# Kernel tuning notes

Hardware: AMD Instinct MI355X
Metric: run time of the kernel (lower is better)

## Reference

```python
import jax, jax.numpy as jnp
import numpy as np

B = 100000          # polymers
MOLS_PER = 4        # 3 monomers + 1 solvent per polymer
N = B * MOLS_PER
D = 64              # rdkit feature dim
F = 64              # polymer-level feature dim
H = 128             # hidden dim


def setup_inputs() -> dict:
    key = jax.random.key(0)
    ks = jax.random.split(key, 6)
    polymer_feats = jax.random.normal(ks[0], (B, F), dtype=jnp.float32)
    rdkit = jax.random.normal(ks[1], (N, D), dtype=jnp.float32)
    # sorted segment ids; last molecule of each segment is the solvent
    polymer_mapping = jnp.repeat(jnp.arange(B, dtype=jnp.int32), MOLS_PER)
    W1 = jax.random.normal(ks[2], (F + 2 * D, H), dtype=jnp.float32) * 0.05
    b1 = jnp.zeros((H,), jnp.float32)
    W2 = jax.random.normal(ks[3], (H, H // 2), dtype=jnp.float32) * 0.05
    b2 = jnp.zeros((H // 2,), jnp.float32)
    W3 = jax.random.normal(ks[4], (H // 2, 1), dtype=jnp.float32) * 0.05
    b3 = jnp.zeros((1,), jnp.float32)
    return {"polymer_feats": polymer_feats, "rdkit": rdkit,
            "polymer_mapping": polymer_mapping,
            "W1": W1, "b1": b1, "W2": W2, "b2": b2, "W3": W3, "b3": b3}


def _combine_rdkit(rdkit, polymer_mapping, num_polymers):
    # solvent = last row of each consecutive segment
    last = jnp.concatenate([polymer_mapping[1:] != polymer_mapping[:-1],
                            jnp.ones((1,), dtype=bool)])
    mono = ~last
    mono_w = mono.astype(rdkit.dtype)
    mono_sum = jax.ops.segment_sum(rdkit * mono_w[:, None], polymer_mapping,
                                   num_segments=num_polymers)
    mono_cnt = jax.ops.segment_sum(mono_w, polymer_mapping,
                                   num_segments=num_polymers)
    mono_avg = mono_sum / mono_cnt[:, None]
    solvent = jax.ops.segment_sum(rdkit * last.astype(rdkit.dtype)[:, None],
                                  polymer_mapping, num_segments=num_polymers)
    return jnp.concatenate([mono_avg, solvent], axis=1)  # [B, 2D]


def reference(polymer_feats, rdkit, polymer_mapping, W1, b1, W2, b2, W3, b3):
    num_polymers = polymer_feats.shape[0]
    pooled = _combine_rdkit(rdkit, polymer_mapping, num_polymers)
    x = jnp.concatenate([polymer_feats, pooled], axis=1)  # [B, F+2D]
    h = jax.nn.relu(x @ W1 + b1)          # dropout is identity in eval mode
    h = jax.nn.relu(h @ W2 + b2)
    return h @ W3 + b3                    # [B, 1]
```

## Files before the change

### kernel.cpp

```cpp
#include <hip/hip_runtime.h>

#define BPOLY  100000
#define TILE_M 64
#define NBLK   ((BPOLY + TILE_M - 1) / TILE_M)
#define KSTR   200

typedef __attribute__((ext_vector_type(8))) _Float16 f16x8;
typedef __attribute__((ext_vector_type(4))) _Float16 f16x4;
typedef __attribute__((ext_vector_type(4))) float    f32x4;

#define W1T 0
#define W2T 24576

__global__ __launch_bounds__(256) void prep_weights(
    const float* __restrict__ W1,
    const float* __restrict__ W2,
    _Float16* __restrict__ ws) {
  int i = blockIdx.x * 256 + threadIdx.x;
  if (i < 24576) {
    int k = i >> 7, n = i & 127;
    ws[W1T + n * 192 + k] = (_Float16)W1[i];
  } else {
    int j = i - 24576;
    int k = j >> 6, n = j & 63;
    ws[W2T + n * 128 + k] = (_Float16)W2[j];
  }
}

__global__ __launch_bounds__(256, 6) void fnn_mfma(
    const float* __restrict__ pf,
    const float* __restrict__ rdkit,
    const _Float16* __restrict__ ws,
    const float* __restrict__ b1,
    const float* __restrict__ b2,
    const float* __restrict__ W3,
    const float* __restrict__ b3,
    float* __restrict__ out) {
  __shared__ __align__(16) _Float16 Xs[64 * KSTR];

  const int tid  = threadIdx.x;
  const int p0   = blockIdx.x * TILE_M;
  const int lane = tid & 63;
  const int wv   = tid >> 6;
  const int lmod = lane & 15;
  const int lq   = lane >> 4;

  #pragma unroll
  for (int i = 0; i < 4; ++i) {
    int f = tid + i * 256;
    int m = f >> 4, kq = (f & 15) * 4;
    float4 v = make_float4(0.f, 0.f, 0.f, 0.f);
    if (p0 + m < BPOLY) v = *(const float4*)(pf + (size_t)(p0 + m) * 64 + kq);
    f16x4 h = {(_Float16)v.x, (_Float16)v.y, (_Float16)v.z, (_Float16)v.w};
    *(f16x4*)&Xs[m * KSTR + kq] = h;
  }
  #pragma unroll
  for (int i = 0; i < 4; ++i) {
    int f = tid + i * 256;
    int m = f >> 4, kq = (f & 15) * 4;
    float4 r0 = {0,0,0,0}, r1 = {0,0,0,0}, r2 = {0,0,0,0}, r3 = {0,0,0,0};
    if (p0 + m < BPOLY) {
      const float* base = rdkit + (size_t)(p0 + m) * 256 + kq;
      r0 = *(const float4*)(base);
      r1 = *(const float4*)(base + 64);
      r2 = *(const float4*)(base + 128);
      r3 = *(const float4*)(base + 192);
    }
    const float inv3 = 1.0f / 3.0f;
    f16x4 av = {(_Float16)((r0.x + r1.x + r2.x) * inv3),
                (_Float16)((r0.y + r1.y + r2.y) * inv3),
                (_Float16)((r0.z + r1.z + r2.z) * inv3),
                (_Float16)((r0.w + r1.w + r2.w) * inv3)};
    f16x4 sv = {(_Float16)r3.x, (_Float16)r3.y, (_Float16)r3.z, (_Float16)r3.w};
    *(f16x4*)&Xs[m * KSTR + 64 + kq]  = av;
    *(f16x4*)&Xs[m * KSTR + 128 + kq] = sv;
  }
  __syncthreads();

  const float b1v0 = b1[32 * wv + lmod];
  const float b1v1 = b1[32 * wv + 16 + lmod];
  const _Float16* w1t = ws + W1T;
  const int bcol0 = (32 * wv + lmod) * 192;
  const int bcol1 = (32 * wv + 16 + lmod) * 192;

  f32x4 acc1[4][2];
  #pragma unroll
  for (int mt = 0; mt < 4; ++mt) {
    acc1[mt][0] = (f32x4){0.f, 0.f, 0.f, 0.f};
    acc1[mt][1] = (f32x4){0.f, 0.f, 0.f, 0.f};
  }

  #pragma unroll 2
  for (int ks = 0; ks < 6; ++ks) {
    const int ko = ks * 32 + lq * 8;
    f16x8 b0 = *(const f16x8*)(w1t + bcol0 + ko);
    f16x8 b1f = *(const f16x8*)(w1t + bcol1 + ko);
    #pragma unroll
    for (int mt = 0; mt < 4; ++mt) {
      f16x8 a = *(const f16x8*)&Xs[(mt * 16 + lmod) * KSTR + ko];
      acc1[mt][0] = __builtin_amdgcn_mfma_f32_16x16x32_f16(a, b0,  acc1[mt][0], 0, 0, 0);
      acc1[mt][1] = __builtin_amdgcn_mfma_f32_16x16x32_f16(a, b1f, acc1[mt][1], 0, 0, 0);
    }
  }
  __syncthreads();

  #pragma unroll
  for (int mt = 0; mt < 4; ++mt) {
    #pragma unroll
    for (int nn = 0; nn < 2; ++nn) {
      const float bv = nn ? b1v1 : b1v0;
      const int col = 32 * wv + 16 * nn + lmod;
      #pragma unroll
      for (int r = 0; r < 4; ++r) {
        float h = fmaxf(acc1[mt][nn][r] + bv, 0.f);
        Xs[(mt * 16 + lq * 4 + r) * KSTR + col] = (_Float16)h;
      }
    }
  }
  __syncthreads();

  const float b2v = b2[16 * wv + lmod];
  const float w3v = W3[16 * wv + lmod];
  const _Float16* w2t = ws + W2T;
  const int bcol2 = (16 * wv + lmod) * 128;

  f32x4 acc2[4];
  #pragma unroll
  for (int mt = 0; mt < 4; ++mt) acc2[mt] = (f32x4){0.f, 0.f, 0.f, 0.f};

  #pragma unroll 2
  for (int ks = 0; ks < 4; ++ks) {
    const int ko = ks * 32 + lq * 8;
    f16x8 b = *(const f16x8*)(w2t + bcol2 + ko);
    #pragma unroll
    for (int mt = 0; mt < 4; ++mt) {
      f16x8 a = *(const f16x8*)&Xs[(mt * 16 + lmod) * KSTR + ko];
      acc2[mt] = __builtin_amdgcn_mfma_f32_16x16x32_f16(a, b, acc2[mt], 0, 0, 0);
    }
  }

  float part[4][4];
  #pragma unroll
  for (int mt = 0; mt < 4; ++mt)
    #pragma unroll
    for (int r = 0; r < 4; ++r)
      part[mt][r] = fmaxf(acc2[mt][r] + b2v, 0.f) * w3v;

  #pragma unroll
  for (int mask = 1; mask <= 8; mask <<= 1)
    #pragma unroll
    for (int mt = 0; mt < 4; ++mt)
      #pragma unroll
      for (int r = 0; r < 4; ++r)
        part[mt][r] += __shfl_xor(part[mt][r], mask);

  if (lmod == 0) {
    #pragma unroll
    for (int mt = 0; mt < 4; ++mt)
      #pragma unroll
      for (int r = 0; r < 4; ++r) {
        int row = mt * 16 + lq * 4 + r;
        *(float*)&Xs[row * KSTR + 128 + 2 * wv] = part[mt][r];
      }
  }
  __syncthreads();

  if (tid < 64) {
    int p = p0 + tid;
    if (p < BPOLY) {
      float4 ps = *(const float4*)&Xs[tid * KSTR + 128];
      out[p] = ps.x + ps.y + ps.z + ps.w + b3[0];
    }
  }
}

extern "C" void kernel_launch(void* const* d_in, const int* in_sizes, int n_in,
                              void* d_out, int out_size, void* d_ws, size_t ws_size,
                              hipStream_t stream) {
  const float* pf    = (const float*)d_in[0];
  const float* rdkit = (const float*)d_in[1];
  const float* W1 = (const float*)d_in[3];
  const float* b1 = (const float*)d_in[4];
  const float* W2 = (const float*)d_in[5];
  const float* b2 = (const float*)d_in[6];
  const float* W3 = (const float*)d_in[7];
  const float* b3 = (const float*)d_in[8];
  _Float16* ws = (_Float16*)d_ws;
  float* out = (float*)d_out;

  prep_weights<<<128, 256, 0, stream>>>(W1, W2, ws);
  fnn_mfma<<<NBLK, 256, 0, stream>>>(pf, rdkit, ws, b1, b2, W3, b3, out);
}
```

Measured before the change: 195.4 us.

## Shrink tile to 48 rows, raise occupancy, prefetch weights, clamp loads

Reduces the per-block row tile from 64 to 48 and raises the launch-bounds occupancy hint from 6 to 8 blocks, shrinking LDS and register use per block so more blocks can be resident to hide the memory latency of streaming rdkit. The weight fragments for both GEMMs are software-prefetched one k-step ahead with fully unrolled loops. Out-of-range row loads are clamped to the last valid row instead of being branched, so loads are unconditional. The cost is more blocks with a larger share of fixed per-block overhead (weight fragment loads, barriers) and fewer MFMAs per weight fetch.

```diff
diff --git a/kernel.cpp b/kernel.cpp
--- a/kernel.cpp
+++ b/kernel.cpp
@@ -1,7 +1,7 @@
 #include <hip/hip_runtime.h>
 
 #define BPOLY  100000
-#define TILE_M 64
+#define TILE_M 48
 #define NBLK   ((BPOLY + TILE_M - 1) / TILE_M)
 #define KSTR   200
 
@@ -27,7 +27,7 @@
   }
 }
 
-__global__ __launch_bounds__(256, 6) void fnn_mfma(
+__global__ __launch_bounds__(256, 8) void fnn_mfma(
     const float* __restrict__ pf,
     const float* __restrict__ rdkit,
     const _Float16* __restrict__ ws,
@@ -36,7 +36,7 @@
     const float* __restrict__ W3,
     const float* __restrict__ b3,
     float* __restrict__ out) {
-  __shared__ __align__(16) _Float16 Xs[64 * KSTR];
+  __shared__ __align__(16) _Float16 Xs[TILE_M * KSTR];
 
   const int tid  = threadIdx.x;
   const int p0   = blockIdx.x * TILE_M;
@@ -45,27 +45,33 @@
   const int lmod = lane & 15;
   const int lq   = lane >> 4;
 
-  #pragma unroll
-  for (int i = 0; i < 4; ++i) {
+  {
+    int f0 = tid, f1 = tid + 256, f2 = tid + 512;
+    int m0 = f0 >> 4, m1 = f1 >> 4, m2 = f2 >> 4;
+    int k0 = (f0 & 15) * 4, k1 = (f1 & 15) * 4, k2 = (f2 & 15) * 4;
+    int q0 = p0 + m0 < BPOLY ? p0 + m0 : BPOLY - 1;
+    int q1 = p0 + m1 < BPOLY ? p0 + m1 : BPOLY - 1;
+    int q2 = p0 + m2 < BPOLY ? p0 + m2 : BPOLY - 1;
+    float4 v0 = *(const float4*)(pf + (size_t)q0 * 64 + k0);
+    float4 v1 = *(const float4*)(pf + (size_t)q1 * 64 + k1);
+    float4 v2 = *(const float4*)(pf + (size_t)q2 * 64 + k2);
+    f16x4 h0 = {(_Float16)v0.x, (_Float16)v0.y, (_Float16)v0.z, (_Float16)v0.w};
+    f16x4 h1 = {(_Float16)v1.x, (_Float16)v1.y, (_Float16)v1.z, (_Float16)v1.w};
+    f16x4 h2 = {(_Float16)v2.x, (_Float16)v2.y, (_Float16)v2.z, (_Float16)v2.w};
+    *(f16x4*)&Xs[m0 * KSTR + k0] = h0;
+    *(f16x4*)&Xs[m1 * KSTR + k1] = h1;
+    *(f16x4*)&Xs[m2 * KSTR + k2] = h2;
+  }
+  #pragma unroll
+  for (int i = 0; i < 3; ++i) {
     int f = tid + i * 256;
     int m = f >> 4, kq = (f & 15) * 4;
-    float4 v = make_float4(0.f, 0.f, 0.f, 0.f);
-    if (p0 + m < BPOLY) v = *(const float4*)(pf + (size_t)(p0 + m) * 64 + kq);
-    f16x4 h = {(_Float16)v.x, (_Float16)v.y, (_Float16)v.z, (_Float16)v.w};
-    *(f16x4*)&Xs[m * KSTR + kq] = h;
-  }
-  #pragma unroll
-  for (int i = 0; i < 4; ++i) {
-    int f = tid + i * 256;
-    int m = f >> 4, kq = (f & 15) * 4;
-    float4 r0 = {0,0,0,0}, r1 = {0,0,0,0}, r2 = {0,0,0,0}, r3 = {0,0,0,0};
-    if (p0 + m < BPOLY) {
-      const float* base = rdkit + (size_t)(p0 + m) * 256 + kq;
-      r0 = *(const float4*)(base);
-      r1 = *(const float4*)(base + 64);
-      r2 = *(const float4*)(base + 128);
-      r3 = *(const float4*)(base + 192);
-    }
+    int q = p0 + m < BPOLY ? p0 + m : BPOLY - 1;
+    const float* base = rdkit + (size_t)q * 256 + kq;
+    float4 r0 = *(const float4*)(base);
+    float4 r1 = *(const float4*)(base + 64);
+    float4 r2 = *(const float4*)(base + 128);
+    float4 r3 = *(const float4*)(base + 192);
     const float inv3 = 1.0f / 3.0f;
     f16x4 av = {(_Float16)((r0.x + r1.x + r2.x) * inv3),
                 (_Float16)((r0.y + r1.y + r2.y) * inv3),
@@ -79,33 +85,36 @@
 
   const float b1v0 = b1[32 * wv + lmod];
   const float b1v1 = b1[32 * wv + 16 + lmod];
-  const _Float16* w1t = ws + W1T;
-  const int bcol0 = (32 * wv + lmod) * 192;
-  const int bcol1 = (32 * wv + 16 + lmod) * 192;
-
-  f32x4 acc1[4][2];
-  #pragma unroll
-  for (int mt = 0; mt < 4; ++mt) {
+  const _Float16* w1n0 = ws + W1T + (32 * wv + lmod) * 192;
+  const _Float16* w1n1 = ws + W1T + (32 * wv + 16 + lmod) * 192;
+
+  f32x4 acc1[3][2];
+  #pragma unroll
+  for (int mt = 0; mt < 3; ++mt) {
     acc1[mt][0] = (f32x4){0.f, 0.f, 0.f, 0.f};
     acc1[mt][1] = (f32x4){0.f, 0.f, 0.f, 0.f};
   }
 
-  #pragma unroll 2
+  f16x8 w0 = *(const f16x8*)(w1n0 + lq * 8);
+  f16x8 w1 = *(const f16x8*)(w1n1 + lq * 8);
+  #pragma unroll
   for (int ks = 0; ks < 6; ++ks) {
+    const int kn = (ks < 5 ? (ks + 1) * 32 : 0) + lq * 8;
+    f16x8 nw0 = *(const f16x8*)(w1n0 + kn);
+    f16x8 nw1 = *(const f16x8*)(w1n1 + kn);
     const int ko = ks * 32 + lq * 8;
-    f16x8 b0 = *(const f16x8*)(w1t + bcol0 + ko);
-    f16x8 b1f = *(const f16x8*)(w1t + bcol1 + ko);
-    #pragma unroll
-    for (int mt = 0; mt < 4; ++mt) {
+    #pragma unroll
+    for (int mt = 0; mt < 3; ++mt) {
       f16x8 a = *(const f16x8*)&Xs[(mt * 16 + lmod) * KSTR + ko];
-      acc1[mt][0] = __builtin_amdgcn_mfma_f32_16x16x32_f16(a, b0,  acc1[mt][0], 0, 0, 0);
-      acc1[mt][1] = __builtin_amdgcn_mfma_f32_16x16x32_f16(a, b1f, acc1[mt][1], 0, 0, 0);
-    }
-  }
-  __syncthreads();
-
-  #pragma unroll
-  for (int mt = 0; mt < 4; ++mt) {
+      acc1[mt][0] = __builtin_amdgcn_mfma_f32_16x16x32_f16(a, w0, acc1[mt][0], 0, 0, 0);
+      acc1[mt][1] = __builtin_amdgcn_mfma_f32_16x16x32_f16(a, w1, acc1[mt][1], 0, 0, 0);
+    }
+    w0 = nw0; w1 = nw1;
+  }
+  __syncthreads();
+
+  #pragma unroll
+  for (int mt = 0; mt < 3; ++mt)
     #pragma unroll
     for (int nn = 0; nn < 2; ++nn) {
       const float bv = nn ? b1v1 : b1v0;
@@ -116,32 +125,33 @@
         Xs[(mt * 16 + lq * 4 + r) * KSTR + col] = (_Float16)h;
       }
     }
-  }
   __syncthreads();
 
   const float b2v = b2[16 * wv + lmod];
   const float w3v = W3[16 * wv + lmod];
-  const _Float16* w2t = ws + W2T;
-  const int bcol2 = (16 * wv + lmod) * 128;
-
-  f32x4 acc2[4];
-  #pragma unroll
-  for (int mt = 0; mt < 4; ++mt) acc2[mt] = (f32x4){0.f, 0.f, 0.f, 0.f};
-
-  #pragma unroll 2
+  const _Float16* w2n = ws + W2T + (16 * wv + lmod) * 128;
+
+  f32x4 acc2[3];
+  #pragma unroll
+  for (int mt = 0; mt < 3; ++mt) acc2[mt] = (f32x4){0.f, 0.f, 0.f, 0.f};
+
+  f16x8 w2f = *(const f16x8*)(w2n + lq * 8);
+  #pragma unroll
   for (int ks = 0; ks < 4; ++ks) {
+    const int kn = (ks < 3 ? (ks + 1) * 32 : 0) + lq * 8;
+    f16x8 nw = *(const f16x8*)(w2n + kn);
     const int ko = ks * 32 + lq * 8;
-    f16x8 b = *(const f16x8*)(w2t + bcol2 + ko);
-    #pragma unroll
-    for (int mt = 0; mt < 4; ++mt) {
+    #pragma unroll
+    for (int mt = 0; mt < 3; ++mt) {
       f16x8 a = *(const f16x8*)&Xs[(mt * 16 + lmod) * KSTR + ko];
-      acc2[mt] = __builtin_amdgcn_mfma_f32_16x16x32_f16(a, b, acc2[mt], 0, 0, 0);
-    }
-  }
-
-  float part[4][4];
-  #pragma unroll
-  for (int mt = 0; mt < 4; ++mt)
+      acc2[mt] = __builtin_amdgcn_mfma_f32_16x16x32_f16(a, w2f, acc2[mt], 0, 0, 0);
+    }
+    w2f = nw;
+  }
+
+  float part[3][4];
+  #pragma unroll
+  for (int mt = 0; mt < 3; ++mt)
     #pragma unroll
     for (int r = 0; r < 4; ++r)
       part[mt][r] = fmaxf(acc2[mt][r] + b2v, 0.f) * w3v;
@@ -149,23 +159,21 @@
   #pragma unroll
   for (int mask = 1; mask <= 8; mask <<= 1)
     #pragma unroll
-    for (int mt = 0; mt < 4; ++mt)
+    for (int mt = 0; mt < 3; ++mt)
       #pragma unroll
       for (int r = 0; r < 4; ++r)
         part[mt][r] += __shfl_xor(part[mt][r], mask);
 
   if (lmod == 0) {
     #pragma unroll
-    for (int mt = 0; mt < 4; ++mt)
+    for (int mt = 0; mt < 3; ++mt)
       #pragma unroll
-      for (int r = 0; r < 4; ++r) {
-        int row = mt * 16 + lq * 4 + r;
-        *(float*)&Xs[row * KSTR + 128 + 2 * wv] = part[mt][r];
-      }
-  }
-  __syncthreads();
-
-  if (tid < 64) {
+      for (int r = 0; r < 4; ++r)
+        *(float*)&Xs[(mt * 16 + lq * 4 + r) * KSTR + 128 + 2 * wv] = part[mt][r];
+  }
+  __syncthreads();
+
+  if (tid < TILE_M) {
     int p = p0 + tid;
     if (p < BPOLY) {
       float4 ps = *(const float4*)&Xs[tid * KSTR + 128];
```

Measured after the change: 189.5 us. 1.03x faster.
